# Kernel tuning notes

Measured on AMD Instinct MI355X. Metric: run time of the kernel, lower is better.

Reference implementation:

```python
import jax, jax.numpy as jnp
import numpy as np

B, T, D, L = 8, 8192, 256, 3
DISTS = (1, 5, 15, 30)


def _layernorm(x, g, b, eps=1e-5):
    m = x.mean(-1, keepdims=True)
    v = ((x - m) ** 2).mean(-1, keepdims=True)
    return (x - m) * jax.lax.rsqrt(v + eps) * g + b


def _temporal_edges():
    src, dst = [], []
    for d in DISTS:
        a = np.arange(T - d)
        src += [a, a + d]
        dst += [a + d, a]
    ei = np.stack([np.concatenate(src), np.concatenate(dst)])  # [2, E]
    off = (np.arange(B) * T).repeat(ei.shape[1])
    return np.tile(ei, (1, B)) + off[None, :]  # [2, B*E]


def setup_inputs() -> dict:
    key = jax.random.key(0)
    ks = jax.random.split(key, 6)
    s = 1.0 / np.sqrt(D)
    s4 = 1.0 / np.sqrt(4 * D)
    return dict(
        x=jax.random.normal(ks[0], (B, T, D), jnp.float32),
        adjacency=jnp.zeros((T, T), jnp.float32),  # shape-check only
        edge_index=jnp.asarray(_temporal_edges(), jnp.int32),
        conv_w=jax.random.normal(ks[1], (L, D, D), jnp.float32) * s,
        conv_b=jnp.zeros((L, D), jnp.float32),
        norm_g=jnp.ones((L, D), jnp.float32),
        norm_b=jnp.zeros((L, D), jnp.float32),
        normff_g=jnp.ones((D,), jnp.float32),
        normff_b=jnp.zeros((D,), jnp.float32),
        w1=jax.random.normal(ks[2], (D, 4 * D), jnp.float32) * s,
        b1=jnp.zeros((4 * D,), jnp.float32),
        w2=jax.random.normal(ks[3], (4 * D, D), jnp.float32) * s4,
        b2=jnp.zeros((D,), jnp.float32),
    )


def reference(x, adjacency, edge_index, conv_w, conv_b, norm_g, norm_b,
              normff_g, normff_b, w1, b1, w2, b2):
    b, t, d = x.shape
    n = b * t
    xf = x.reshape(n, d)
    src, dst = edge_index[0], edge_index[1]
    # GCN symmetric degree normalization (no self loops), degrees by target node
    deg = jax.ops.segment_sum(jnp.ones(src.shape[0], x.dtype), dst, num_segments=n)
    dinv = jnp.where(deg > 0, jax.lax.rsqrt(deg), 0.0)
    enorm = (dinv[src] * dinv[dst])[:, None]  # [E,1]
    for i in range(conv_w.shape[0]):
        h = xf @ conv_w[i]                                    # [N,D]
        h = jax.ops.segment_sum(h[src] * enorm, dst, num_segments=n) + conv_b[i]
        h = jax.nn.gelu(h, approximate=False)
        h = _layernorm(h.reshape(b, t, d), norm_g[i], norm_b[i]).reshape(n, d)
        xf = xf + h
    x = xf.reshape(b, t, d)
    y = _layernorm(x, normff_g, normff_b)
    ff = jax.nn.gelu(y @ w1 + b1, approximate=False) @ w2 + b2
    return x + ff
```

## Files before the change

kernel.cpp:

```cpp
#include <hip/hip_runtime.h>
#include <hip/hip_bf16.h>
#include <math.h>
#include <stdint.h>
#include <stddef.h>

#define TB 8
#define TT 8192
#define DD 256
#define NR (TB * TT)
#define HH 1024
#define LL 3

typedef unsigned short ushort_t;
typedef __attribute__((ext_vector_type(8))) short short8;
typedef __attribute__((ext_vector_type(4))) float floatx4;

__device__ __forceinline__ float bf2f(ushort_t u) {
  union { unsigned int i; float f; } x; x.i = ((unsigned int)u) << 16; return x.f;
}
__device__ __forceinline__ ushort_t f2bf(float f) {
  union { float f; unsigned int i; } x; x.f = f;
  unsigned int r = x.i + 0x7fffu + ((x.i >> 16) & 1u);
  return (ushort_t)(r >> 16);
}
__device__ __forceinline__ float ld_in(const void* p, size_t i, int isf) {
  return isf ? ((const float*)p)[i] : bf2f(((const ushort_t*)p)[i]);
}
__device__ __forceinline__ float gelu_f(float v) {
  const float y = v * (0.7978845608028654f + 0.035677408136300125f * v * v);
  const float e = __expf(-2.0f * y);
  return v * __builtin_amdgcn_rcpf(1.0f + e);
}
__device__ __forceinline__ int deg_of(int t) {
  return (t >= 1) + (t >= 5) + (t >= 15) + (t >= 30)
       + (t < TT - 1) + (t < TT - 5) + (t < TT - 15) + (t < TT - 30);
}
__device__ __forceinline__ void gl_lds16(const ushort_t* g, void* l) {
  __builtin_amdgcn_global_load_lds(
      (const __attribute__((address_space(1))) unsigned int*)(g),
      (__attribute__((address_space(3))) unsigned int*)(l), 16, 0, 0);
}
__device__ __forceinline__ int xcd_swz(int lin, int nwg) {
  const int q = nwg >> 3;
  return (lin & 7) * q + (lin >> 3);
}
__device__ __forceinline__ int swz128(int row, int bytecol) {
  return row * 128 + (bytecol ^ ((row & 7) << 4));
}
__device__ __forceinline__ int swz64(int row, int bytecol) {
  return row * 64 + (bytecol ^ ((row & 3) << 4));
}
#define WAIT_VM0()  asm volatile("s_waitcnt vmcnt(0)" ::: "memory")
#define WAIT_VM4()  asm volatile("s_waitcnt vmcnt(4)" ::: "memory")
#define WAIT_LGKM0() asm volatile("s_waitcnt lgkmcnt(0)" ::: "memory")

__global__ void k_probe(const void* __restrict__ x, int* __restrict__ flag) {
  if (threadIdx.x == 0 && blockIdx.x == 0) {
    const float* fb = (const float*)x;
    int okf = 0;
    for (int i = 0; i < 128; ++i) {
      const float av = fabsf(fb[i]);
      if (av > 1e-6f && av < 100.f) okf++;
    }
    *flag = (okf >= 115) ? 1 : 0;
  }
}

__device__ __forceinline__ void transpose_tile(
    char* smem_, const void* cw, const void* w1, const void* w2,
    ushort_t* cwT, ushort_t* w1T, ushort_t* w2T, int isf, int b, int tid) {
  ushort_t (*tile)[33] = (ushort_t(*)[33])smem_;
  const void* src; ushort_t* dst; int R, C, bx, by; size_t row0;
  if (b < 192) {
    const int i = b >> 6, t = b & 63;
    src = cw; dst = cwT + (size_t)i * DD * DD; row0 = (size_t)i * DD;
    R = DD; C = DD; bx = (t & 7) * 32; by = (t >> 3) * 32;
  } else if (b < 448) {
    const int t = b - 192;
    src = w1; dst = w1T; row0 = 0; R = DD; C = HH;
    bx = (t & 31) * 32; by = (t >> 5) * 32;
  } else {
    const int t = b - 448;
    src = w2; dst = w2T; row0 = 0; R = HH; C = DD;
    bx = (t & 7) * 32; by = (t >> 3) * 32;
  }
  const int tx = tid & 31, ty = tid >> 5;
  __syncthreads();
  for (int i = ty; i < 32; i += 8)
    tile[i][tx] = f2bf(ld_in(src, (row0 + by + i) * (size_t)C + bx + tx, isf));
  __syncthreads();
  for (int i = ty; i < 32; i += 8)
    dst[(size_t)(bx + i) * R + by + tx] = tile[tx][i];
}

__global__ __launch_bounds__(256) void k_phase0(
    const void* __restrict__ x, ushort_t* __restrict__ xA,
    const void* __restrict__ cw, const void* __restrict__ w1,
    const void* __restrict__ w2, ushort_t* __restrict__ cwT,
    ushort_t* __restrict__ w1T, ushort_t* __restrict__ w2T,
    const int* __restrict__ flag) {
  __shared__ alignas(16) char smem[4224];
  const int isf = *flag;
  const int bid = blockIdx.x, tid = threadIdx.x;
  transpose_tile(smem, cw, w1, w2, cwT, w1T, w2T, isf, bid, tid);
  if (bid < 192)
    transpose_tile(smem, cw, w1, w2, cwT, w1T, w2T, isf, 512 + bid, tid);
  const size_t c0 = (size_t)bid * 8192 + tid;
  if (isf) {
    const float4* xf = (const float4*)x;
    ushort4* xo = (ushort4*)xA;
#pragma unroll
    for (int i = 0; i < 32; ++i) {
      const float4 f = xf[c0 + i * 256];
      ushort4 u; u.x = f2bf(f.x); u.y = f2bf(f.y); u.z = f2bf(f.z); u.w = f2bf(f.w);
      xo[c0 + i * 256] = u;
    }
  } else {
#pragma unroll
    for (int i = 0; i < 32; ++i)
      ((ushort4*)xA)[c0 + i * 256] = ((const ushort4*)x)[c0 + i * 256];
  }
}

__global__ __launch_bounds__(256, 2) void k_conv_fused(
    const ushort_t* __restrict__ xin, ushort_t* __restrict__ xout,
    const ushort_t* __restrict__ Bt, const void* __restrict__ bias,
    size_t boff, const void* __restrict__ g, const void* __restrict__ bn,
    size_t goff, const int* __restrict__ flag) {
  __shared__ alignas(16) char smem[68096];
  float* scr    = (float*)smem;
  float* part   = scr;
  float* partsq = scr + 256;
  float* smu    = scr + 512;
  float* srs    = scr + 576;
  char* aggA    = smem + 2560;
  char* rt      = smem + 2560;
  const int isf = *flag;

  const int tid  = threadIdx.x;
  const int lane = tid & 63;
  const int l16  = lane & 15;
  const int quad = lane >> 4;
  const int w    = tid >> 6;
  const int m0   = xcd_swz(blockIdx.x, gridDim.x) * 64;

  char* lB = smem + 35328 + w * 8192;

  const int srow = lane >> 3;
  const int sseg = (lane & 7) ^ (srow & 7);
  auto stageB = [&](int kc) {
#pragma unroll
    for (int i = 0; i < 8; ++i)
      gl_lds16(Bt + (size_t)(w * 64 + i * 8 + srow) * DD + kc * 64 + sseg * 8,
               lB + i * 1024);
  };
  stageB(0);

  const int tbase = m0 & (TT - 1);
  const bool interior = (tbase >= 60) && (tbase <= TT - 124);
  const int koffs[8] = {-30, -15, -5, -1, 1, 5, 15, 30};
#pragma unroll
  for (int j = 0; j < 8; ++j) {
    const int id = j * 256 + tid;
    const int r = id >> 5, c = id & 31;
    const ushort_t* base = xin + (size_t)(m0 + r) * DD + c * 8;
    float s[8] = {0.f, 0.f, 0.f, 0.f, 0.f, 0.f, 0.f, 0.f};
    if (interior) {
#pragma unroll
      for (int e = 0; e < 8; ++e) {
        const short8 u = *(const short8*)(base + (ptrdiff_t)koffs[e] * DD);
#pragma unroll
        for (int q2 = 0; q2 < 8; ++q2) s[q2] += bf2f((ushort_t)u[q2]);
      }
#pragma unroll
      for (int q2 = 0; q2 < 8; ++q2) s[q2] *= 0.125f;
    } else {
      const int t = tbase + r;
      const float di = rsqrtf((float)deg_of(t));
#pragma unroll
      for (int e = 0; e < 8; ++e) {
        const int t2 = t + koffs[e];
        if ((unsigned)t2 < (unsigned)TT) {
          const float wgt = di * rsqrtf((float)deg_of(t2));
          const short8 u = *(const short8*)(base + (ptrdiff_t)koffs[e] * DD);
#pragma unroll
          for (int q2 = 0; q2 < 8; ++q2) s[q2] += wgt * bf2f((ushort_t)u[q2]);
        }
      }
    }
    short8 o;
#pragma unroll
    for (int q2 = 0; q2 < 8; ++q2) o[q2] = (short)f2bf(s[q2]);
    *(short8*)(aggA + (c >> 3) * 8192 + swz128(r, (c & 7) * 16)) = o;
  }
  WAIT_LGKM0();
  __builtin_amdgcn_s_barrier();
  __builtin_amdgcn_sched_barrier(0);

  floatx4 acc[4][4];
#pragma unroll
  for (int i = 0; i < 4; ++i)
#pragma unroll
    for (int j = 0; j < 4; ++j) acc[i][j] = {0.f, 0.f, 0.f, 0.f};

#pragma unroll
  for (int kc = 0; kc < 4; ++kc) {
    WAIT_VM0();
    short8 af0[4], bf0[4], af1[4], bf1[4];
#pragma unroll
    for (int mt = 0; mt < 4; ++mt) {
      af0[mt] = *(const short8*)(aggA + kc * 8192 +
                   swz128(mt * 16 + l16, quad * 16));
      af1[mt] = *(const short8*)(aggA + kc * 8192 +
                   swz128(mt * 16 + l16, 64 + quad * 16));
    }
#pragma unroll
    for (int nt = 0; nt < 4; ++nt) {
      bf0[nt] = *(const short8*)(lB + swz128(nt * 16 + l16, quad * 16));
      bf1[nt] = *(const short8*)(lB + swz128(nt * 16 + l16, 64 + quad * 16));
    }
    WAIT_LGKM0();
    __builtin_amdgcn_sched_barrier(0);
    if (kc < 3) stageB(kc + 1);
    __builtin_amdgcn_s_setprio(1);
#pragma unroll
    for (int mt = 0; mt < 4; ++mt)
#pragma unroll
      for (int nt = 0; nt < 4; ++nt)
        acc[mt][nt] = __builtin_amdgcn_mfma_f32_16x16x32_bf16(
            af0[mt], bf0[nt], acc[mt][nt], 0, 0, 0);
#pragma unroll
    for (int mt = 0; mt < 4; ++mt)
#pragma unroll
      for (int nt = 0; nt < 4; ++nt)
        acc[mt][nt] = __builtin_amdgcn_mfma_f32_16x16x32_bf16(
            af1[mt], bf1[nt], acc[mt][nt], 0, 0, 0);
    __builtin_amdgcn_s_setprio(0);
  }

#pragma unroll
  for (int nt = 0; nt < 4; ++nt) {
    const float bv = ld_in(bias, boff + w * 64 + nt * 16 + l16, isf);
#pragma unroll
    for (int mt = 0; mt < 4; ++mt)
#pragma unroll
      for (int r = 0; r < 4; ++r)
        acc[mt][nt][r] = gelu_f(acc[mt][nt][r] + bv);
  }
#pragma unroll
  for (int mt = 0; mt < 4; ++mt) {
#pragma unroll
    for (int r = 0; r < 4; ++r) {
      float p = 0.f, q = 0.f;
#pragma unroll
      for (int nt = 0; nt < 4; ++nt) {
        const float v = acc[mt][nt][r];
        p += v; q += v * v;
      }
#pragma unroll
      for (int o = 8; o > 0; o >>= 1) {
        p += __shfl_xor(p, o, 64);
        q += __shfl_xor(q, o, 64);
      }
      if (l16 == 0) {
        const int rowloc = mt * 16 + quad * 4 + r;
        part[w * 64 + rowloc] = p;
        partsq[w * 64 + rowloc] = q;
      }
    }
  }
  __syncthreads();
  if (tid < 64) {
    const float s  = part[tid] + part[64 + tid] + part[128 + tid] + part[192 + tid];
    const float sq = partsq[tid] + partsq[64 + tid] + partsq[128 + tid] + partsq[192 + tid];
    const float mu = s * (1.0f / DD);
    const float var = sq * (1.0f / DD) - mu * mu;
    smu[tid] = mu;
    srs[tid] = rsqrtf(var + 1e-5f);
  }
  __syncthreads();

#pragma unroll
  for (int nt = 0; nt < 4; ++nt) {
    const int col = w * 64 + nt * 16 + l16;
    const float gv = ld_in(g, goff + col, isf);
    const float bnv = ld_in(bn, goff + col, isf);
#pragma unroll
    for (int mt = 0; mt < 4; ++mt) {
#pragma unroll
      for (int r = 0; r < 4; ++r) {
        const int rowloc = mt * 16 + quad * 4 + r;
        *(ushort_t*)(rt + (rowloc * 264 + col) * 2) =
            f2bf((acc[mt][nt][r] - smu[rowloc]) * srs[rowloc] * gv + bnv);
      }
    }
  }
  __syncthreads();

#pragma unroll
  for (int i = 0; i < 8; ++i) {
    const int ch = tid + i * 256;
    const int row = ch >> 5, sg = ch & 31;
    const short8 xv = *(const short8*)(xin + (size_t)(m0 + row) * DD + sg * 8);
    const short8 rv = *(const short8*)(rt + (row * 264 + sg * 8) * 2);
    short8 ov;
#pragma unroll
    for (int j = 0; j < 8; ++j)
      ov[j] = (short)f2bf(bf2f((ushort_t)xv[j]) + bf2f((ushort_t)rv[j]));
    __builtin_nontemporal_store(
        ov, (short8*)(xout + (size_t)(m0 + row) * DD + sg * 8));
  }
}

__global__ __launch_bounds__(256, 2) void k_ffn(
    const ushort_t* __restrict__ xb, const ushort_t* __restrict__ w1T,
    const ushort_t* __restrict__ w2T, const void* __restrict__ gff,
    const void* __restrict__ bff, const void* __restrict__ b1,
    const void* __restrict__ b2, void* __restrict__ dout,
    const int* __restrict__ flag) {
  __shared__ alignas(16) char smem[81920];
  char* An = smem;
  char* Zs = smem + 32768;
  char* Rs = smem;
  const int isf = *flag;

  const int tid  = threadIdx.x;
  const int lane = tid & 63;
  const int l16  = lane & 15;
  const int quad = lane >> 4;
  const int w    = tid >> 6;
  const int m0   = xcd_swz(blockIdx.x, gridDim.x) * 64;
  char* Bw0 = smem + 49152 + w * 8192;

  const int sr8 = lane >> 3;
  const int ss8 = (lane & 7) ^ (sr8 & 7);
  const int sr4 = lane >> 2;
  const int ss4 = (lane & 3) ^ (sr4 & 3);

  auto stage_g = [&](int gg) {
    if (gg >= 64) return;
    const int n1 = gg >> 3, s = gg & 7;
    char* dst = Bw0 + (gg & 1) * 4096;
    if (s < 4) {
#pragma unroll
      for (int i = 0; i < 4; ++i)
        gl_lds16(w1T + (size_t)(n1 * 128 + w * 32 + i * 8 + sr8) * DD +
                     s * 64 + ss8 * 8,
                 dst + i * 1024);
    } else {
      const int kc2 = (s - 4) >> 1, ks = (s - 4) & 1;
#pragma unroll
      for (int i = 0; i < 4; ++i)
        gl_lds16(w2T + (size_t)(w * 64 + i * 16 + sr4) * HH +
                     n1 * 128 + kc2 * 64 + ks * 32 + ss4 * 8,
                 dst + i * 1024);
    }
  };

  stage_g(0);
  stage_g(1);

  const int sg = tid & 31;
  float gffv[8], bffv[8];
#pragma unroll
  for (int j = 0; j < 8; ++j) {
    gffv[j] = ld_in(gff, sg * 8 + j, isf);
    bffv[j] = ld_in(bff, sg * 8 + j, isf);
  }
#pragma unroll
  for (int i = 0; i < 8; ++i) {
    const int row = (tid + i * 256) >> 5;
    const short8 xv = *(const short8*)(xb + (size_t)(m0 + row) * DD + sg * 8);
    float v[8], ps = 0.f, pq = 0.f;
#pragma unroll
    for (int j = 0; j < 8; ++j) {
      v[j] = bf2f((ushort_t)xv[j]); ps += v[j]; pq += v[j] * v[j];
    }
#pragma unroll
    for (int o = 16; o > 0; o >>= 1) {
      ps += __shfl_xor(ps, o, 64);
      pq += __shfl_xor(pq, o, 64);
    }
    const float mu = ps * (1.0f / DD);
    const float rs = rsqrtf(pq * (1.0f / DD) - mu * mu + 1e-5f);
    short8 o8;
#pragma unroll
    for (int j = 0; j < 8; ++j)
      o8[j] = (short)f2bf((v[j] - mu) * rs * gffv[j] + bffv[j]);
    *(short8*)(An + (sg >> 3) * 8192 + swz128(row, (sg & 7) * 16)) = o8;
  }
  WAIT_LGKM0();
  __builtin_amdgcn_s_barrier();
  __builtin_amdgcn_sched_barrier(0);

  floatx4 acc2[4][4];
#pragma unroll
  for (int i = 0; i < 4; ++i)
#pragma unroll
    for (int j = 0; j < 4; ++j) acc2[i][j] = {0.f, 0.f, 0.f, 0.f};

  for (int n1 = 0; n1 < 8; ++n1) {
    const float b1v0 = ld_in(b1, n1 * 128 + w * 32 + l16, isf);
    const float b1v1 = ld_in(b1, n1 * 128 + w * 32 + 16 + l16, isf);

    floatx4 acc1[4][2];
#pragma unroll
    for (int i = 0; i < 4; ++i)
#pragma unroll
      for (int j = 0; j < 2; ++j) acc1[i][j] = {0.f, 0.f, 0.f, 0.f};

#pragma unroll
    for (int kc = 0; kc < 4; ++kc) {
      const int gs = n1 * 8 + kc;
      WAIT_VM4();
      const char* Bw = Bw0 + (gs & 1) * 4096;
      short8 af0[4], af1[4], bq0[2], bq1[2];
#pragma unroll
      for (int mt = 0; mt < 4; ++mt) {
        af0[mt] = *(const short8*)(An + kc * 8192 +
                     swz128(mt * 16 + l16, quad * 16));
        af1[mt] = *(const short8*)(An + kc * 8192 +
                     swz128(mt * 16 + l16, 64 + quad * 16));
      }
#pragma unroll
      for (int nt = 0; nt < 2; ++nt) {
        bq0[nt] = *(const short8*)(Bw + swz128(nt * 16 + l16, quad * 16));
        bq1[nt] = *(const short8*)(Bw + swz128(nt * 16 + l16, 64 + quad * 16));
      }
      WAIT_LGKM0();
      __builtin_amdgcn_sched_barrier(0);
      stage_g(gs + 2);
      __builtin_amdgcn_s_setprio(1);
#pragma unroll
      for (int mt = 0; mt < 4; ++mt)
#pragma unroll
        for (int nt = 0; nt < 2; ++nt)
          acc1[mt][nt] = __builtin_amdgcn_mfma_f32_16x16x32_bf16(
              af0[mt], bq0[nt], acc1[mt][nt], 0, 0, 0);
#pragma unroll
      for (int mt = 0; mt < 4; ++mt)
#pragma unroll
        for (int nt = 0; nt < 2; ++nt)
          acc1[mt][nt] = __builtin_amdgcn_mfma_f32_16x16x32_bf16(
              af1[mt], bq1[nt], acc1[mt][nt], 0, 0, 0);
      __builtin_amdgcn_s_setprio(0);
    }

#pragma unroll
    for (int nt = 0; nt < 2; ++nt) {
      const int col = w * 32 + nt * 16 + l16;
      const float b1v = nt ? b1v1 : b1v0;
#pragma unroll
      for (int mt = 0; mt < 4; ++mt)
#pragma unroll
        for (int r = 0; r < 4; ++r) {
          const int row = mt * 16 + quad * 4 + r;
          *(ushort_t*)(Zs + (col >> 6) * 8192 + swz128(row, (col & 63) * 2)) =
              f2bf(gelu_f(acc1[mt][nt][r] + b1v));
        }
    }
    WAIT_LGKM0();
    __builtin_amdgcn_s_barrier();
    __builtin_amdgcn_sched_barrier(0);

#pragma unroll
    for (int s2 = 0; s2 < 4; ++s2) {
      const int gs = n1 * 8 + 4 + s2;
      const int kc2 = s2 >> 1, ks = s2 & 1;
      if (gs == 63) { WAIT_VM0(); } else { WAIT_VM4(); }
      const char* Bw = Bw0 + (gs & 1) * 4096;
      short8 af[4], bfr[4];
#pragma unroll
      for (int mt = 0; mt < 4; ++mt)
        af[mt] = *(const short8*)(Zs + kc2 * 8192 +
                   swz128(mt * 16 + l16, ks * 64 + quad * 16));
#pragma unroll
      for (int nt = 0; nt < 4; ++nt)
        bfr[nt] = *(const short8*)(Bw + swz64(nt * 16 + l16, quad * 16));
      WAIT_LGKM0();
      __builtin_amdgcn_sched_barrier(0);
      stage_g(gs + 2);
      __builtin_amdgcn_s_setprio(1);
#pragma unroll
      for (int mt = 0; mt < 4; ++mt)
#pragma unroll
        for (int nt = 0; nt < 4; ++nt)
          acc2[mt][nt] = __builtin_amdgcn_mfma_f32_16x16x32_bf16(
              af[mt], bfr[nt], acc2[mt][nt], 0, 0, 0);
      __builtin_amdgcn_s_setprio(0);
    }
    __builtin_amdgcn_s_barrier();
    __builtin_amdgcn_sched_barrier(0);
  }

#pragma unroll
  for (int i = 0; i < 8; ++i)
    gl_lds16(xb + (size_t)(m0 + ((i * 256 + tid) >> 5)) * DD +
                 ((i * 256 + tid) & 31) * 8,
             Rs + i * 4096 + w * 1024);
  __syncthreads();

#pragma unroll
  for (int nt = 0; nt < 4; ++nt) {
    const int col = w * 64 + nt * 16 + l16;
    const float b2v = ld_in(b2, col, isf);
#pragma unroll
    for (int mt = 0; mt < 4; ++mt) {
#pragma unroll
      for (int r = 0; r < 4; ++r) {
        const int lr = mt * 16 + quad * 4 + r;
        const float v = acc2[mt][nt][r] + b2v +
                        bf2f(*(const ushort_t*)(Rs + lr * 512 + col * 2));
        const size_t idx = (size_t)(m0 + lr) * DD + col;
        if (isf) __builtin_nontemporal_store(v, &((float*)dout)[idx]);
        else     __builtin_nontemporal_store(f2bf(v), &((ushort_t*)dout)[idx]);
      }
    }
  }
}

extern "C" void kernel_launch(void* const* d_in, const int* in_sizes, int n_in,
                              void* d_out, int out_size, void* d_ws, size_t ws_size,
                              hipStream_t stream) {
  const void* x      = d_in[0];
  const void* conv_w = d_in[3];
  const void* conv_b = d_in[4];
  const void* norm_g = d_in[5];
  const void* norm_b = d_in[6];
  const void* nff_g  = d_in[7];
  const void* nff_b  = d_in[8];
  const void* w1     = d_in[9];
  const void* b1     = d_in[10];
  const void* w2     = d_in[11];
  const void* b2     = d_in[12];
  (void)in_sizes; (void)n_in; (void)out_size; (void)ws_size;

  char* ws = (char*)d_ws;
  int*      flag = (int*)ws;      ws += 16;
  ushort_t* xA   = (ushort_t*)ws; ws += (size_t)NR * DD * 2;
  ushort_t* xB   = (ushort_t*)ws; ws += (size_t)NR * DD * 2;
  ushort_t* cwT  = (ushort_t*)ws; ws += (size_t)LL * DD * DD * 2;
  ushort_t* w1T  = (ushort_t*)ws; ws += (size_t)DD * HH * 2;
  ushort_t* w2T  = (ushort_t*)ws; ws += (size_t)HH * DD * 2;

  k_probe<<<1, 64, 0, stream>>>(x, flag);
  k_phase0<<<512, 256, 0, stream>>>(x, xA, conv_w, w1, w2, cwT, w1T, w2T,
                                    flag);

  k_conv_fused<<<NR / 64, 256, 0, stream>>>(
      xA, xB, cwT, conv_b, 0, norm_g, norm_b, 0, flag);
  k_conv_fused<<<NR / 64, 256, 0, stream>>>(
      xB, xA, cwT + (size_t)DD * DD, conv_b, DD, norm_g, norm_b, DD, flag);
  k_conv_fused<<<NR / 64, 256, 0, stream>>>(
      xA, xB, cwT + (size_t)2 * DD * DD, conv_b, 2 * DD, norm_g, norm_b,
      2 * DD, flag);

  k_ffn<<<NR / 64, 256, 0, stream>>>(
      xB, w1T, w2T, nff_g, nff_b, b1, b2, d_out, flag);
}
```

Before: 640.2 us.

## Halve conv weight staging buffer to fit three blocks per CU

The graph-conv kernel now stages the weight tile in 32-wide K slices (8 stages) instead of 64-wide slices (4 stages). This halves the per-wave LDS staging buffer, which lowers total shared memory enough to raise the launch bound to 3 blocks per CU and hide more latency. It also drops the MFMA priority bump and replaces the nontemporal output store with a plain store. In exchange there are more barrier-like waits per K step, the reduced ILP per iteration risks exposing staging latency, and register pressure rises under the tighter occupancy target.

```diff
diff --git a/kernel.cpp b/kernel.cpp
--- a/kernel.cpp
+++ b/kernel.cpp
@@ -122,12 +122,12 @@
   }
 }
 
-__global__ __launch_bounds__(256, 2) void k_conv_fused(
+__global__ __launch_bounds__(256, 3) void k_conv_fused(
     const ushort_t* __restrict__ xin, ushort_t* __restrict__ xout,
     const ushort_t* __restrict__ Bt, const void* __restrict__ bias,
     size_t boff, const void* __restrict__ g, const void* __restrict__ bn,
     size_t goff, const int* __restrict__ flag) {
-  __shared__ alignas(16) char smem[68096];
+  __shared__ alignas(16) char smem[51712];
   float* scr    = (float*)smem;
   float* part   = scr;
   float* partsq = scr + 256;
@@ -144,14 +144,16 @@
   const int w    = tid >> 6;
   const int m0   = xcd_swz(blockIdx.x, gridDim.x) * 64;
 
-  char* lB = smem + 35328 + w * 8192;
-
-  const int srow = lane >> 3;
-  const int sseg = (lane & 7) ^ (srow & 7);
-  auto stageB = [&](int kc) {
-#pragma unroll
-    for (int i = 0; i < 8; ++i)
-      gl_lds16(Bt + (size_t)(w * 64 + i * 8 + srow) * DD + kc * 64 + sseg * 8,
+  char* lB = smem + 35328 + w * 4096;
+
+  const int sr4 = lane >> 2;
+  const int ss4 = (lane & 3) ^ (sr4 & 3);
+  auto stageB = [&](int s) {
+    const int kc = s >> 1, ks = s & 1;
+#pragma unroll
+    for (int i = 0; i < 4; ++i)
+      gl_lds16(Bt + (size_t)(w * 64 + i * 16 + sr4) * DD +
+                   kc * 64 + ks * 32 + ss4 * 8,
                lB + i * 1024);
   };
   stageB(0);
@@ -204,38 +206,26 @@
     for (int j = 0; j < 4; ++j) acc[i][j] = {0.f, 0.f, 0.f, 0.f};
 
 #pragma unroll
-  for (int kc = 0; kc < 4; ++kc) {
+  for (int s = 0; s < 8; ++s) {
     WAIT_VM0();
-    short8 af0[4], bf0[4], af1[4], bf1[4];
-#pragma unroll
-    for (int mt = 0; mt < 4; ++mt) {
-      af0[mt] = *(const short8*)(aggA + kc * 8192 +
-                   swz128(mt * 16 + l16, quad * 16));
-      af1[mt] = *(const short8*)(aggA + kc * 8192 +
-                   swz128(mt * 16 + l16, 64 + quad * 16));
-    }
-#pragma unroll
-    for (int nt = 0; nt < 4; ++nt) {
-      bf0[nt] = *(const short8*)(lB + swz128(nt * 16 + l16, quad * 16));
-      bf1[nt] = *(const short8*)(lB + swz128(nt * 16 + l16, 64 + quad * 16));
-    }
+    const int kc = s >> 1, ks = s & 1;
+    short8 af[4], bfr[4];
+#pragma unroll
+    for (int mt = 0; mt < 4; ++mt)
+      af[mt] = *(const short8*)(aggA + kc * 8192 +
+                 swz128(mt * 16 + l16, ks * 64 + quad * 16));
+#pragma unroll
+    for (int nt = 0; nt < 4; ++nt)
+      bfr[nt] = *(const short8*)(lB + swz64(nt * 16 + l16, quad * 16));
     WAIT_LGKM0();
     __builtin_amdgcn_sched_barrier(0);
-    if (kc < 3) stageB(kc + 1);
-    __builtin_amdgcn_s_setprio(1);
+    if (s < 7) stageB(s + 1);
 #pragma unroll
     for (int mt = 0; mt < 4; ++mt)
 #pragma unroll
       for (int nt = 0; nt < 4; ++nt)
         acc[mt][nt] = __builtin_amdgcn_mfma_f32_16x16x32_bf16(
-            af0[mt], bf0[nt], acc[mt][nt], 0, 0, 0);
-#pragma unroll
-    for (int mt = 0; mt < 4; ++mt)
-#pragma unroll
-      for (int nt = 0; nt < 4; ++nt)
-        acc[mt][nt] = __builtin_amdgcn_mfma_f32_16x16x32_bf16(
-            af1[mt], bf1[nt], acc[mt][nt], 0, 0, 0);
-    __builtin_amdgcn_s_setprio(0);
+            af[mt], bfr[nt], acc[mt][nt], 0, 0, 0);
   }
 
 #pragma unroll
@@ -307,8 +297,7 @@
 #pragma unroll
     for (int j = 0; j < 8; ++j)
       ov[j] = (short)f2bf(bf2f((ushort_t)xv[j]) + bf2f((ushort_t)rv[j]));
-    __builtin_nontemporal_store(
-        ov, (short8*)(xout + (size_t)(m0 + row) * DD + sg * 8));
+    *(short8*)(xout + (size_t)(m0 + row) * DD + sg * 8) = ov;
   }
 }
 
```

New measurement: 656.6 us. +2.6%, slower.
